# Optimization experiments

Measured on AMD Instinct MI355X. Metric: run time of the kernel, lower is better.

## Reference

```python
import jax, jax.numpy as jnp
import numpy as np

B, S, D, H = 4, 2048, 1024, 16
HD = D // H


def setup_inputs() -> dict:
    key = jax.random.key(0)
    ks = jax.random.split(key, 5)
    scale = 0.02
    return {
        "x": jax.random.normal(ks[0], (B, S, D), dtype=jnp.float32),
        "Wq": jax.random.normal(ks[1], (D, D), dtype=jnp.float32) * scale,
        "Wk": jax.random.normal(ks[2], (D, D), dtype=jnp.float32) * scale,
        "Wv": jax.random.normal(ks[3], (D, D), dtype=jnp.float32) * scale,
        "Wo": jax.random.normal(ks[4], (D, D), dtype=jnp.float32) * scale,
    }


def reference(x, Wq, Wk, Wv, Wo):
    b, s, d = x.shape
    # Linear layers (torch Linear: y = x @ W.T), no bias
    q = jnp.einsum('bsd,ed->bse', x, Wq).reshape(b, s, H, HD).transpose(0, 2, 1, 3)
    k = jnp.einsum('bsd,ed->bse', x, Wk).reshape(b, s, H, HD).transpose(0, 2, 1, 3)
    v = jnp.einsum('bsd,ed->bse', x, Wv).reshape(b, s, H, HD).transpose(0, 2, 1, 3)
    # [B,H,S,S] attention scores
    scores = jnp.einsum('bhqd,bhkd->bhqk', q, k)
    causal = jnp.tril(jnp.ones((s, s), dtype=bool))
    scores = jnp.where(causal, scores, -jnp.inf)
    # faithful to source: mask first, then scale, then softmax
    weights = jax.nn.softmax(scores / jnp.sqrt(jnp.float32(HD)), axis=-1)
    # dropout p=0.0 (eval): identity
    ctx = jnp.einsum('bhqk,bhkd->bhqd', weights, v)
    ctx = ctx.transpose(0, 2, 1, 3).reshape(b, s, d)
    return jnp.einsum('bsd,ed->bse', ctx, Wo)
```

## Files before the change

kernel.cpp:

```cpp
#include <hip/hip_runtime.h>
#include <math.h>

typedef unsigned short u16;
typedef __attribute__((ext_vector_type(8))) short short8;
typedef __attribute__((ext_vector_type(4))) float f32x4;

constexpr int Bb = 4, S_LEN = 2048, DMODEL = 1024, NH = 16;
constexpr int MTOT = Bb * S_LEN;

#define QSCALE 0.18033688011112042f

__device__ __forceinline__ u16 f2bf(float f) {
    union { float f; unsigned u; } v; v.f = f;
    unsigned r = v.u + 0x7FFFu + ((v.u >> 16) & 1u);
    return (u16)(r >> 16);
}

__device__ __forceinline__ float exp2_fast(float x) {
#if __has_builtin(__builtin_amdgcn_exp2f)
    return __builtin_amdgcn_exp2f(x);
#else
    float r; asm("v_exp_f32 %0, %1" : "=v"(r) : "v"(x)); return r;
#endif
}

__device__ __forceinline__ void load_lds16(const void* g, void* l) {
    __builtin_amdgcn_global_load_lds(
        (const __attribute__((address_space(1))) unsigned int*)g,
        (__attribute__((address_space(3))) unsigned int*)l, 16, 0, 0);
}

__global__ __launch_bounds__(256)
void cvt_all(const float* __restrict__ x,
             const float* __restrict__ w0, const float* __restrict__ w1,
             const float* __restrict__ w2, const float* __restrict__ w3,
             u16* __restrict__ xb, u16* __restrict__ b0, u16* __restrict__ b1,
             u16* __restrict__ b2, u16* __restrict__ b3)
{
    int gid = blockIdx.x * 256 + threadIdx.x;
    constexpr int NXo = (MTOT * DMODEL) / 8;
    constexpr int NWo = (DMODEL * DMODEL) / 8;
    const float* s; u16* d; int o;
    float sc = 1.0f;
    if (gid < NXo) { s = x; d = xb; o = gid; }
    else {
        int t = gid - NXo;
        int w = t >> 17;
        o = t & (NWo - 1);
        s = (w == 0) ? w0 : (w == 1) ? w1 : (w == 2) ? w2 : w3;
        d = (w == 0) ? b0 : (w == 1) ? b1 : (w == 2) ? b2 : b3;
        if (w == 0) sc = QSCALE;
    }
    const float4* sp = (const float4*)(s + (size_t)o * 8);
    float4 a = sp[0], bq = sp[1];
    short8 ov;
    ov[0] = (short)f2bf(a.x * sc);  ov[1] = (short)f2bf(a.y * sc);
    ov[2] = (short)f2bf(a.z * sc);  ov[3] = (short)f2bf(a.w * sc);
    ov[4] = (short)f2bf(bq.x * sc); ov[5] = (short)f2bf(bq.y * sc);
    ov[6] = (short)f2bf(bq.z * sc); ov[7] = (short)f2bf(bq.w * sc);
    *(short8*)(d + (size_t)o * 8) = ov;
}

__global__ __launch_bounds__(256, 2)
void gemm_bt(const u16* __restrict__ X,
             const u16* __restrict__ W0, const u16* __restrict__ W1, const u16* __restrict__ W2,
             u16* __restrict__ Y0, u16* __restrict__ Y1, u16* __restrict__ Y2,
             int M, int N, int K)
{
    const u16* W = (blockIdx.z == 0) ? W0 : (blockIdx.z == 1) ? W1 : W2;
    u16*       Y = (blockIdx.z == 0) ? Y0 : (blockIdx.z == 1) ? Y1 : Y2;

    __shared__ __align__(16) u16 lA[128 * 64];
    __shared__ __align__(16) u16 lB[128 * 64];

    const int tid  = threadIdx.x;
    const int wave = tid >> 6;
    const int lane = tid & 63;
    const int qd   = lane >> 4;
    const int c    = lane & 15;
    const int tm   = blockIdx.x * 128;
    const int tn   = blockIdx.y * 128;
    const int wm   = (wave >> 1) * 64;
    const int wn   = (wave & 1) * 64;

    f32x4 acc[4][4] = {};

    for (int k0 = 0; k0 < K; k0 += 64) {
        if (k0) __syncthreads();
#pragma unroll
        for (int it = 0; it < 4; ++it) {
            int chunk = it * 256 + tid;
            int row = chunk >> 3, hc = chunk & 7;
            load_lds16(X + (size_t)(tm + row) * K + k0 + hc * 8,
                       (char*)lA + (it * 256 + wave * 64) * 16);
            load_lds16(W + (size_t)(tn + row) * K + k0 + hc * 8,
                       (char*)lB + (it * 256 + wave * 64) * 16);
        }
        __syncthreads();

#pragma unroll
        for (int kk = 0; kk < 64; kk += 32) {
            short8 a[4], b[4];
#pragma unroll
            for (int i = 0; i < 4; ++i) {
                a[i] = *(const short8*)&lA[(wm + i * 16 + c) * 64 + kk + qd * 8];
                b[i] = *(const short8*)&lB[(wn + i * 16 + c) * 64 + kk + qd * 8];
            }
#pragma unroll
            for (int mi = 0; mi < 4; ++mi)
#pragma unroll
                for (int ni = 0; ni < 4; ++ni)
                    acc[mi][ni] = __builtin_amdgcn_mfma_f32_16x16x32_bf16(
                        a[mi], b[ni], acc[mi][ni], 0, 0, 0);
        }
    }

#pragma unroll
    for (int mi = 0; mi < 4; ++mi)
#pragma unroll
        for (int ni = 0; ni < 4; ++ni)
#pragma unroll
            for (int r = 0; r < 4; ++r) {
                int row = tm + wm + mi * 16 + qd * 4 + r;
                int col = tn + wn + ni * 16 + c;
                Y[(size_t)row * N + col] = f2bf(acc[mi][ni][r]);
            }
}

__global__ __launch_bounds__(256, 2)
void gemm_bt_f32(const u16* __restrict__ X, const u16* __restrict__ W,
                 float* __restrict__ Y, int M, int N, int K)
{
    __shared__ __align__(16) u16 lA[128 * 64];
    __shared__ __align__(16) u16 lB[128 * 64];

    const int tid  = threadIdx.x;
    const int wave = tid >> 6;
    const int lane = tid & 63;
    const int qd   = lane >> 4;
    const int c    = lane & 15;
    const int tm   = blockIdx.x * 128;
    const int tn   = blockIdx.y * 128;
    const int wm   = (wave >> 1) * 64;
    const int wn   = (wave & 1) * 64;

    f32x4 acc[4][4] = {};

    for (int k0 = 0; k0 < K; k0 += 64) {
        if (k0) __syncthreads();
#pragma unroll
        for (int it = 0; it < 4; ++it) {
            int chunk = it * 256 + tid;
            int row = chunk >> 3, hc = chunk & 7;
            load_lds16(X + (size_t)(tm + row) * K + k0 + hc * 8,
                       (char*)lA + (it * 256 + wave * 64) * 16);
            load_lds16(W + (size_t)(tn + row) * K + k0 + hc * 8,
                       (char*)lB + (it * 256 + wave * 64) * 16);
        }
        __syncthreads();

#pragma unroll
        for (int kk = 0; kk < 64; kk += 32) {
            short8 a[4], b[4];
#pragma unroll
            for (int i = 0; i < 4; ++i) {
                a[i] = *(const short8*)&lA[(wm + i * 16 + c) * 64 + kk + qd * 8];
                b[i] = *(const short8*)&lB[(wn + i * 16 + c) * 64 + kk + qd * 8];
            }
#pragma unroll
            for (int mi = 0; mi < 4; ++mi)
#pragma unroll
                for (int ni = 0; ni < 4; ++ni)
                    acc[mi][ni] = __builtin_amdgcn_mfma_f32_16x16x32_bf16(
                        a[mi], b[ni], acc[mi][ni], 0, 0, 0);
        }
    }

#pragma unroll
    for (int mi = 0; mi < 4; ++mi)
#pragma unroll
        for (int ni = 0; ni < 4; ++ni)
#pragma unroll
            for (int r = 0; r < 4; ++r) {
                int row = tm + wm + mi * 16 + qd * 4 + r;
                int col = tn + wn + ni * 16 + c;
                Y[(size_t)row * N + col] = acc[mi][ni][r];
            }
}

__global__ __launch_bounds__(256)
void transpose_v(const u16* __restrict__ V, u16* __restrict__ VT)
{
    const int sblk = blockIdx.x;
    const int bh   = blockIdx.y;
    const int b = bh >> 4, h = bh & 15;
    __shared__ __align__(16) u16 lT[64][72];

    const int t = threadIdx.x;
#pragma unroll
    for (int it = 0; it < 2; ++it) {
        int chunk = it * 256 + t;
        int si = chunk >> 3, hc = chunk & 7;
        short8 val = *(const short8*)&V[(size_t)(b * S_LEN + sblk * 64 + si) * DMODEL + h * 64 + hc * 8];
        *(short8*)&lT[si][hc * 8] = val;
    }
    __syncthreads();
#pragma unroll
    for (int it = 0; it < 2; ++it) {
        int chunk = it * 256 + t;
        int hd = chunk >> 3, sc = chunk & 7;
        short8 o;
#pragma unroll
        for (int j = 0; j < 8; ++j) o[j] = (short)lT[sc * 8 + j][hd];
        *(short8*)&VT[(size_t)(bh * 64 + hd) * S_LEN + sblk * 64 + sc * 8] = o;
    }
}

__global__ __launch_bounds__(512, 4)
void attention(const u16* __restrict__ Q, const u16* __restrict__ K,
               const u16* __restrict__ VT, u16* __restrict__ CTX)
{
    const int p  = blockIdx.x;
    const int bh = blockIdx.y;
    const int b = bh >> 4, h = bh & 15;

    __shared__ __align__(16) u16 lK[2][64 * 64];
    __shared__ __align__(16) u16 lV[2][64 * 64];
    __shared__ __align__(16) u16 lP[128 * 72];

    const int tid = threadIdx.x, wave = tid >> 6, lane = tid & 63;
    const int qd = lane >> 4, c = lane & 15;
    const int wrow = wave * 16;
    const int srow = tid >> 3, shc = tid & 7;
    const int shcs = shc ^ (srow & 7);
    const int rx   = c & 7;
    const size_t kbase = (size_t)(b * S_LEN) * DMODEL + h * 64;
    const size_t vbase = (size_t)(bh * 64) * S_LEN;

#pragma unroll
    for (int phase = 0; phase < 2; ++phase) {
        const int qt = phase ? (15 - p) : p;
        const int q0 = qt * 128;
        const int nkv = 2 * qt + 2;

        short8 qf[2];
#pragma unroll
        for (int ks = 0; ks < 2; ++ks)
            qf[ks] = *(const short8*)&Q[(size_t)(b * S_LEN + q0 + wrow + c) * DMODEL
                                        + h * 64 + ks * 32 + qd * 8];

        f32x4 oacc[4] = {};
        float psum[4] = {};

        __syncthreads();
        load_lds16(K + kbase + (size_t)srow * DMODEL + shcs * 8,
                   (char*)lK[0] + wave * 1024);
        load_lds16(VT + vbase + (size_t)srow * S_LEN + shcs * 8,
                   (char*)lV[0] + wave * 1024);

        for (int kt = 0; kt < nkv; ++kt) {
            const int cur = kt & 1;
            const int k0 = kt * 64;
            __syncthreads();

            if (kt + 1 < nkv) {
                const int kn = (kt + 1) * 64;
                load_lds16(K + kbase + (size_t)(kn + srow) * DMODEL + shcs * 8,
                           (char*)lK[cur ^ 1] + wave * 1024);
                load_lds16(VT + vbase + (size_t)srow * S_LEN + kn + shcs * 8,
                           (char*)lV[cur ^ 1] + wave * 1024);
            }

            f32x4 sacc[4] = {};
#pragma unroll
            for (int ks = 0; ks < 2; ++ks) {
                short8 kf[4];
#pragma unroll
                for (int ni = 0; ni < 4; ++ni)
                    kf[ni] = *(const short8*)&lK[cur][(ni * 16 + c) * 64
                                                      + (((ks * 4 + qd) ^ rx) << 3)];
#pragma unroll
                for (int ni = 0; ni < 4; ++ni)
                    sacc[ni] = __builtin_amdgcn_mfma_f32_16x16x32_bf16(
                        qf[ks], kf[ni], sacc[ni], 0, 0, 0);
            }

            const bool need_mask = (k0 + 63 > q0);
#pragma unroll
            for (int ni = 0; ni < 4; ++ni) {
                float pv[4];
#pragma unroll
                for (int r = 0; r < 4; ++r) {
                    float t = sacc[ni][r];
                    if (need_mask) {
                        int colg = k0 + ni * 16 + c;
                        int rowg = q0 + wrow + qd * 4 + r;
                        if (colg > rowg) t = -1.0e38f;
                    }
                    t = fminf(t, 86.0f);
                    pv[r] = exp2_fast(t);
                    psum[r] += pv[r];
                }
#pragma unroll
                for (int r = 0; r < 4; r += 2) {
                    unsigned pk;
                    asm("v_cvt_pk_bf16_f32 %0, %1, %2"
                        : "=v"(pk) : "v"(pv[r]), "v"(pv[r + 1]));
                    int base = (wrow + qd * 4 + r) * 72 + ni * 16 + c;
                    lP[base]      = (u16)(pk & 0xffffu);
                    lP[base + 72] = (u16)(pk >> 16);
                }
            }

            asm volatile("s_waitcnt lgkmcnt(0)" ::: "memory");

#pragma unroll
            for (int ks2 = 0; ks2 < 2; ++ks2) {
                short8 af, bf[4];
                af = *(const short8*)&lP[(wrow + c) * 72 + ks2 * 32 + qd * 8];
#pragma unroll
                for (int ni = 0; ni < 4; ++ni)
                    bf[ni] = *(const short8*)&lV[cur][(ni * 16 + c) * 64
                                                      + (((ks2 * 4 + qd) ^ rx) << 3)];
#pragma unroll
                for (int ni = 0; ni < 4; ++ni)
                    oacc[ni] = __builtin_amdgcn_mfma_f32_16x16x32_bf16(
                        af, bf[ni], oacc[ni], 0, 0, 0);
            }
        }

        float linv[4];
#pragma unroll
        for (int r = 0; r < 4; ++r) {
            float l = psum[r];
#pragma unroll
            for (int d = 1; d < 16; d <<= 1) l += __shfl_xor(l, d);
            linv[r] = 1.0f / l;
        }
#pragma unroll
        for (int ni = 0; ni < 4; ++ni)
#pragma unroll
            for (int r = 0; r < 4; ++r) {
                int row = q0 + wrow + qd * 4 + r;
                CTX[(size_t)(b * S_LEN + row) * DMODEL + h * 64 + ni * 16 + c]
                    = f2bf(oacc[ni][r] * linv[r]);
            }
    }
}

extern "C" void kernel_launch(void* const* d_in, const int* in_sizes, int n_in,
                              void* d_out, int out_size, void* d_ws, size_t ws_size,
                              hipStream_t stream)
{
    const size_t MB = 1024 * 1024;
    char* ws = (char*)d_ws;
    if (ws_size < 72 * MB + 64) return;

    u16* xb  = (u16*)ws;
    u16* wb0 = (u16*)(ws + 16 * MB);
    u16* wb1 = (u16*)(ws + 18 * MB);
    u16* wb2 = (u16*)(ws + 20 * MB);
    u16* wb3 = (u16*)(ws + 22 * MB);
    u16* q   = (u16*)(ws + 24 * MB);
    u16* k   = (u16*)(ws + 40 * MB);
    u16* v   = (u16*)(ws + 56 * MB);
    u16* vt  = xb;
    u16* ctx = v;
    float* out = (float*)d_out;

    constexpr int NCVT = (MTOT * DMODEL + 4 * DMODEL * DMODEL) / 8 / 256;

    cvt_all<<<NCVT, 256, 0, stream>>>(
        (const float*)d_in[0], (const float*)d_in[1], (const float*)d_in[2],
        (const float*)d_in[3], (const float*)d_in[4], xb, wb0, wb1, wb2, wb3);

    gemm_bt<<<dim3(MTOT / 128, DMODEL / 128, 3), 256, 0, stream>>>(
        xb, wb0, wb1, wb2, q, k, v, MTOT, DMODEL, DMODEL);
    transpose_v<<<dim3(S_LEN / 64, Bb * NH), 256, 0, stream>>>(v, vt);
    attention<<<dim3(8, Bb * NH), 512, 0, stream>>>(q, k, vt, ctx);
    gemm_bt_f32<<<dim3(MTOT / 128, DMODEL / 128, 1), 256, 0, stream>>>(
        ctx, wb3, out, MTOT, DMODEL, DMODEL);
}
```

Baseline: 261.3 us.

## Switch attention to 32x32 MFMA with register-resident P via lane shuffles

The attention kernel now uses 32x32x16 bf16 MFMAs, computing S^T so the probability tile stays in registers and is rearranged into the A operand with cross-half-wave shuffles. This removes the LDS round trip for P. Each wave now handles 32 query rows, so the query tile grows to 256 and the grid halves. Waves whose rows lie entirely above the causal diagonal skip the KV tile. In exchange, register pressure rises (launch bounds drop to 2 blocks per CU), and fewer blocks may hurt load balance and occupancy.

```diff
diff --git a/kernel.cpp b/kernel.cpp
--- a/kernel.cpp
+++ b/kernel.cpp
@@ -4,6 +4,8 @@
 typedef unsigned short u16;
 typedef __attribute__((ext_vector_type(8))) short short8;
 typedef __attribute__((ext_vector_type(4))) float f32x4;
+typedef __attribute__((ext_vector_type(16))) float f32x16;
+typedef __attribute__((ext_vector_type(4))) unsigned int u32x4;
 
 constexpr int Bb = 4, S_LEN = 2048, DMODEL = 1024, NH = 16;
 constexpr int MTOT = Bb * S_LEN;
@@ -216,7 +218,7 @@
     }
 }
 
-__global__ __launch_bounds__(512, 4)
+__global__ __launch_bounds__(512, 2)
 void attention(const u16* __restrict__ Q, const u16* __restrict__ K,
                const u16* __restrict__ VT, u16* __restrict__ CTX)
 {
@@ -226,31 +228,31 @@
 
     __shared__ __align__(16) u16 lK[2][64 * 64];
     __shared__ __align__(16) u16 lV[2][64 * 64];
-    __shared__ __align__(16) u16 lP[128 * 72];
 
     const int tid = threadIdx.x, wave = tid >> 6, lane = tid & 63;
-    const int qd = lane >> 4, c = lane & 15;
-    const int wrow = wave * 16;
+    const int l31 = lane & 31, hi = lane >> 5;
+    const int wrow = wave * 32;
     const int srow = tid >> 3, shc = tid & 7;
     const int shcs = shc ^ (srow & 7);
-    const int rx   = c & 7;
+    const int rxk  = l31 & 7;
     const size_t kbase = (size_t)(b * S_LEN) * DMODEL + h * 64;
     const size_t vbase = (size_t)(bh * 64) * S_LEN;
 
 #pragma unroll
     for (int phase = 0; phase < 2; ++phase) {
-        const int qt = phase ? (15 - p) : p;
-        const int q0 = qt * 128;
-        const int nkv = 2 * qt + 2;
-
-        short8 qf[2];
-#pragma unroll
-        for (int ks = 0; ks < 2; ++ks)
-            qf[ks] = *(const short8*)&Q[(size_t)(b * S_LEN + q0 + wrow + c) * DMODEL
-                                        + h * 64 + ks * 32 + qd * 8];
-
-        f32x4 oacc[4] = {};
-        float psum[4] = {};
+        const int qt = phase ? (7 - p) : p;
+        const int q0 = qt * 256;
+        const int nkv = 4 * qt + 4;
+        const int qrg = q0 + wrow + l31;
+
+        short8 qf[4];
+#pragma unroll
+        for (int ks = 0; ks < 4; ++ks)
+            qf[ks] = *(const short8*)&Q[(size_t)(b * S_LEN + qrg) * DMODEL
+                                        + h * 64 + ks * 16 + hi * 8];
+
+        f32x16 oacc0 = {}, oacc1 = {};
+        float psum = 0.f;
 
         __syncthreads();
         load_lds16(K + kbase + (size_t)srow * DMODEL + shcs * 8,
@@ -271,80 +273,99 @@
                            (char*)lV[cur ^ 1] + wave * 1024);
             }
 
-            f32x4 sacc[4] = {};
-#pragma unroll
-            for (int ks = 0; ks < 2; ++ks) {
-                short8 kf[4];
-#pragma unroll
-                for (int ni = 0; ni < 4; ++ni)
-                    kf[ni] = *(const short8*)&lK[cur][(ni * 16 + c) * 64
-                                                      + (((ks * 4 + qd) ^ rx) << 3)];
-#pragma unroll
-                for (int ni = 0; ni < 4; ++ni)
-                    sacc[ni] = __builtin_amdgcn_mfma_f32_16x16x32_bf16(
-                        qf[ks], kf[ni], sacc[ni], 0, 0, 0);
-            }
-
-            const bool need_mask = (k0 + 63 > q0);
-#pragma unroll
-            for (int ni = 0; ni < 4; ++ni) {
-                float pv[4];
-#pragma unroll
-                for (int r = 0; r < 4; ++r) {
-                    float t = sacc[ni][r];
-                    if (need_mask) {
-                        int colg = k0 + ni * 16 + c;
-                        int rowg = q0 + wrow + qd * 4 + r;
-                        if (colg > rowg) t = -1.0e38f;
+            if (k0 <= q0 + wrow + 31) {
+                f32x16 s0 = {}, s1 = {};
+#pragma unroll
+                for (int hs = 0; hs < 4; ++hs) {
+                    const int sl = ((hs * 2 + hi) ^ rxk) << 3;
+                    short8 kf0 = *(const short8*)&lK[cur][l31 * 64 + sl];
+                    short8 kf1 = *(const short8*)&lK[cur][(32 + l31) * 64 + sl];
+                    s0 = __builtin_amdgcn_mfma_f32_32x32x16_bf16(kf0, qf[hs], s0, 0, 0, 0);
+                    s1 = __builtin_amdgcn_mfma_f32_32x32x16_bf16(kf1, qf[hs], s1, 0, 0, 0);
+                }
+
+                float pva[16], pvb[16];
+                if (k0 + 63 > q0 + wrow) {
+                    const int lim = qrg - k0 - 4 * hi;
+#pragma unroll
+                    for (int r = 0; r < 16; ++r) {
+                        const int ka = (r & 3) + 8 * (r >> 2);
+                        pva[r] = (ka > lim)      ? -1.0e38f : s0[r];
+                        pvb[r] = (ka + 32 > lim) ? -1.0e38f : s1[r];
                     }
-                    t = fminf(t, 86.0f);
-                    pv[r] = exp2_fast(t);
-                    psum[r] += pv[r];
+                } else {
+#pragma unroll
+                    for (int r = 0; r < 16; ++r) { pva[r] = s0[r]; pvb[r] = s1[r]; }
                 }
 #pragma unroll
-                for (int r = 0; r < 4; r += 2) {
-                    unsigned pk;
+                for (int r = 0; r < 16; ++r) {
+                    pva[r] = exp2_fast(fminf(pva[r], 86.0f));
+                    pvb[r] = exp2_fast(fminf(pvb[r], 86.0f));
+                    psum += pva[r] + pvb[r];
+                }
+                unsigned own0[8], own1[8];
+#pragma unroll
+                for (int q = 0; q < 8; ++q) {
                     asm("v_cvt_pk_bf16_f32 %0, %1, %2"
-                        : "=v"(pk) : "v"(pv[r]), "v"(pv[r + 1]));
-                    int base = (wrow + qd * 4 + r) * 72 + ni * 16 + c;
-                    lP[base]      = (u16)(pk & 0xffffu);
-                    lP[base + 72] = (u16)(pk >> 16);
+                        : "=v"(own0[q]) : "v"(pva[2 * q]), "v"(pva[2 * q + 1]));
+                    asm("v_cvt_pk_bf16_f32 %0, %1, %2"
+                        : "=v"(own1[q]) : "v"(pvb[2 * q]), "v"(pvb[2 * q + 1]));
                 }
-            }
-
-            asm volatile("s_waitcnt lgkmcnt(0)" ::: "memory");
-
-#pragma unroll
-            for (int ks2 = 0; ks2 < 2; ++ks2) {
-                short8 af, bf[4];
-                af = *(const short8*)&lP[(wrow + c) * 72 + ks2 * 32 + qd * 8];
-#pragma unroll
-                for (int ni = 0; ni < 4; ++ni)
-                    bf[ni] = *(const short8*)&lV[cur][(ni * 16 + c) * 64
-                                                      + (((ks2 * 4 + qd) ^ rx) << 3)];
-#pragma unroll
-                for (int ni = 0; ni < 4; ++ni)
-                    oacc[ni] = __builtin_amdgcn_mfma_f32_16x16x32_bf16(
-                        af, bf[ni], oacc[ni], 0, 0, 0);
-            }
-        }
-
-        float linv[4];
-#pragma unroll
-        for (int r = 0; r < 4; ++r) {
-            float l = psum[r];
-#pragma unroll
-            for (int d = 1; d < 16; d <<= 1) l += __shfl_xor(l, d);
-            linv[r] = 1.0f / l;
-        }
-#pragma unroll
-        for (int ni = 0; ni < 4; ++ni)
-#pragma unroll
-            for (int r = 0; r < 4; ++r) {
-                int row = q0 + wrow + qd * 4 + r;
-                CTX[(size_t)(b * S_LEN + row) * DMODEL + h * 64 + ni * 16 + c]
-                    = f2bf(oacc[ni][r] * linv[r]);
-            }
+
+                unsigned r0a = __shfl_xor((int)(hi ? own0[0] : own0[2]), 32);
+                unsigned r0b = __shfl_xor((int)(hi ? own0[1] : own0[3]), 32);
+                unsigned r0c = __shfl_xor((int)(hi ? own0[4] : own0[6]), 32);
+                unsigned r0d = __shfl_xor((int)(hi ? own0[5] : own0[7]), 32);
+                unsigned r1a = __shfl_xor((int)(hi ? own1[0] : own1[2]), 32);
+                unsigned r1b = __shfl_xor((int)(hi ? own1[1] : own1[3]), 32);
+                unsigned r1c = __shfl_xor((int)(hi ? own1[4] : own1[6]), 32);
+                unsigned r1d = __shfl_xor((int)(hi ? own1[5] : own1[7]), 32);
+                unsigned o0a = hi ? own0[2] : own0[0];
+                unsigned o0b = hi ? own0[3] : own0[1];
+                unsigned o0c = hi ? own0[6] : own0[4];
+                unsigned o0d = hi ? own0[7] : own0[5];
+                unsigned o1a = hi ? own1[2] : own1[0];
+                unsigned o1b = hi ? own1[3] : own1[1];
+                unsigned o1c = hi ? own1[6] : own1[4];
+                unsigned o1d = hi ? own1[7] : own1[5];
+
+                u32x4 w0, w1, w2, w3;
+                w0[0] = hi ? r0a : o0a; w0[1] = hi ? r0b : o0b;
+                w0[2] = hi ? o0a : r0a; w0[3] = hi ? o0b : r0b;
+                w1[0] = hi ? r0c : o0c; w1[1] = hi ? r0d : o0d;
+                w1[2] = hi ? o0c : r0c; w1[3] = hi ? o0d : r0d;
+                w2[0] = hi ? r1a : o1a; w2[1] = hi ? r1b : o1b;
+                w2[2] = hi ? o1a : r1a; w2[3] = hi ? o1b : r1b;
+                w3[0] = hi ? r1c : o1c; w3[1] = hi ? r1d : o1d;
+                w3[2] = hi ? o1c : r1c; w3[3] = hi ? o1d : r1d;
+                short8 pa0 = __builtin_bit_cast(short8, w0);
+                short8 pa1 = __builtin_bit_cast(short8, w1);
+                short8 pa2 = __builtin_bit_cast(short8, w2);
+                short8 pa3 = __builtin_bit_cast(short8, w3);
+
+#pragma unroll
+                for (int ks = 0; ks < 4; ++ks) {
+                    const short8 paf = (ks == 0) ? pa0 : (ks == 1) ? pa1
+                                     : (ks == 2) ? pa2 : pa3;
+                    const int vsl = ((ks * 2 + hi) ^ rxk) << 3;
+                    short8 vf0 = *(const short8*)&lV[cur][l31 * 64 + vsl];
+                    short8 vf1 = *(const short8*)&lV[cur][(32 + l31) * 64 + vsl];
+                    oacc0 = __builtin_amdgcn_mfma_f32_32x32x16_bf16(paf, vf0, oacc0, 0, 0, 0);
+                    oacc1 = __builtin_amdgcn_mfma_f32_32x32x16_bf16(paf, vf1, oacc1, 0, 0, 0);
+                }
+            }
+        }
+
+        float pt = psum + __shfl_xor(psum, 32);
+#pragma unroll
+        for (int r = 0; r < 16; ++r) {
+            const int orow = (r & 3) + 8 * (r >> 2) + 4 * hi;
+            float inv = 1.0f / __shfl(pt, orow);
+            const int rowg = q0 + wrow + orow;
+            size_t base = (size_t)(b * S_LEN + rowg) * DMODEL + h * 64;
+            CTX[base + l31]      = f2bf(oacc0[r] * inv);
+            CTX[base + 32 + l31] = f2bf(oacc1[r] * inv);
+        }
     }
 }
 
@@ -377,7 +398,7 @@
     gemm_bt<<<dim3(MTOT / 128, DMODEL / 128, 3), 256, 0, stream>>>(
         xb, wb0, wb1, wb2, q, k, v, MTOT, DMODEL, DMODEL);
     transpose_v<<<dim3(S_LEN / 64, Bb * NH), 256, 0, stream>>>(v, vt);
-    attention<<<dim3(8, Bb * NH), 512, 0, stream>>>(q, k, vt, ctx);
+    attention<<<dim3(4, Bb * NH), 512, 0, stream>>>(q, k, vt, ctx);
     gemm_bt_f32<<<dim3(MTOT / 128, DMODEL / 128, 1), 256, 0, stream>>>(
         ctx, wb3, out, MTOT, DMODEL, DMODEL);
 }
```

New measurement: 261.4 us. About the same (+0.1%).
